# Performance work log

Hardware: AMD Instinct MI355X
Metric: run time of the kernel (lower is better)

Reference implementation:

```python
import jax, jax.numpy as jnp
import numpy as np

N = 100000   # nodes
E = 1600000  # edges (avg degree 16)
H = 128      # hidden_dim
G = 256      # graphs in batch
IN = 2       # input feature dim (GCNConv(2, hidden_dim))


def setup_inputs() -> dict:
    key = jax.random.key(0)
    ks = jax.random.split(key, 12)
    def lin(k, fan_in, shape):
        # kaiming-uniform-ish init, scale irrelevant for correctness testing
        return jax.random.uniform(k, shape, jnp.float32, -1.0, 1.0) / np.sqrt(fan_in).astype(np.float32)
    return {
        "x": jax.random.normal(ks[0], (N, IN), jnp.float32),
        "edge_src": jax.random.randint(ks[1], (E,), 0, N, jnp.int32),
        "edge_dst": jax.random.randint(ks[2], (E,), 0, N, jnp.int32),
        "batch_ids": jnp.sort(jax.random.randint(ks[3], (N,), 0, G, jnp.int32)),
        "num_graphs": G,
        "W1": lin(ks[4], IN, (IN, H)), "b1": jnp.zeros((H,), jnp.float32),
        "W2": lin(ks[5], H, (H, H)),  "b2": jnp.zeros((H,), jnp.float32),
        "fc1_W": lin(ks[6], H, (H, H)), "fc1_b": lin(ks[7], H, (H,)),
        "fc2_W": lin(ks[8], H, (H, 1)), "fc2_b": lin(ks[9], H, (1,)),
    }


def gcn_layer(x, W, b, src, dst, n):
    # PyG GCNConv: add self-loops, symmetric deg^{-1/2} normalization,
    # linear transform, scatter-add aggregation, bias.
    h = x @ W                                                     # [N, H]
    deg = jax.ops.segment_sum(jnp.ones_like(src, jnp.float32), dst, num_segments=n) + 1.0  # +1 self-loop
    dinv = jax.lax.rsqrt(deg)                                     # [N]
    norm = dinv[src] * dinv[dst]                                  # [E]
    agg = jax.ops.segment_sum(h[src] * norm[:, None], dst, num_segments=n)  # [N, H]
    # self-loop contribution: deg_i^{-1/2} * deg_i^{-1/2} = 1/deg_i
    return agg + h * (1.0 / deg)[:, None] + b


def reference(x, edge_src, edge_dst, batch_ids, num_graphs,
              W1, b1, W2, b2, fc1_W, fc1_b, fc2_W, fc2_b):
    n = x.shape[0]
    h = jax.nn.relu(gcn_layer(x, W1, b1, edge_src, edge_dst, n))
    h = jax.nn.relu(gcn_layer(h, W2, b2, edge_src, edge_dst, n))
    # global_mean_pool
    sums = jax.ops.segment_sum(h, batch_ids, num_segments=num_graphs)            # [G, H]
    cnt = jax.ops.segment_sum(jnp.ones((n,), jnp.float32), batch_ids, num_segments=num_graphs)
    pooled = sums / jnp.maximum(cnt, 1.0)[:, None]
    h = jax.nn.relu(pooled @ fc1_W + fc1_b)
    return h @ fc2_W + fc2_b                                                     # [G, 1]
```

## Files before the change

### kernel.cpp

```cpp
#include <hip/hip_runtime.h>
#include <stdint.h>

#define HD 128
#define BSH 9
#define BNODES 512
#define PER 8
#define SCAP 256

typedef float f32x4 __attribute__((ext_vector_type(4)));
typedef float f32x2 __attribute__((ext_vector_type(2)));
typedef short s16x8 __attribute__((ext_vector_type(8)));

static inline int idiv(int a, int b) { return (a + b - 1) / b; }

__device__ __forceinline__ unsigned short f2b(float f) {
  unsigned u = __float_as_uint(f);
  return (unsigned short)((u + 0x7fffu + ((u >> 16) & 1u)) >> 16);
}

__global__ void __launch_bounds__(256) k_cnt(const int* __restrict__ edst,
                                             int* __restrict__ btot,
                                             int E, int NB, int chunk) {
  __shared__ int hist[512];
  int blk = blockIdx.x;
  for (int b = threadIdx.x; b < NB; b += 256) hist[b] = 0;
  __syncthreads();
  int s0 = blk * chunk, s1 = min(E, s0 + chunk);
  for (int k = s0 + threadIdx.x; k < s1; k += 256)
    atomicAdd(&hist[edst[k] >> BSH], 1);
  __syncthreads();
  for (int b = threadIdx.x; b < NB; b += 256) {
    int h = hist[b];
    if (h) atomicAdd(&btot[b], h);
  }
}

__global__ void __launch_bounds__(1024) k_bscan(const int* __restrict__ btot,
                                                int* __restrict__ bstart,
                                                int* __restrict__ gcur,
                                                float4* __restrict__ td,
                                                int NB, int E, int N) {
  __shared__ int sh[1024];
  int t = threadIdx.x;
  int a0 = (2 * t < NB) ? btot[2 * t] : 0;
  int a1 = (2 * t + 1 < NB) ? btot[2 * t + 1] : 0;
  int s = a0 + a1;
  sh[t] = s;
  __syncthreads();
  for (int off = 1; off < 1024; off <<= 1) {
    int add = (t >= off) ? sh[t - off] : 0;
    __syncthreads();
    sh[t] += add;
    __syncthreads();
  }
  int excl = sh[t] - s;
  if (2 * t < NB) { bstart[2 * t] = excl; gcur[2 * t] = excl; }
  if (2 * t + 1 < NB) { bstart[2 * t + 1] = excl + a0; gcur[2 * t + 1] = excl + a0; }
  if (t == 0) {
    bstart[NB] = E;
    td[N] = make_float4(0.f, 0.f, 0.f, 0.f);
  }
}

__global__ void __launch_bounds__(256) k_binscatter2(const int* __restrict__ esrc,
                                                     const int* __restrict__ edst,
                                                     int* __restrict__ gcur,
                                                     unsigned* __restrict__ recs,
                                                     int E, int NB, int chunk) {
  __shared__ int hist[512];
  int blk = blockIdx.x;
  for (int b = threadIdx.x; b < NB; b += 256) hist[b] = 0;
  __syncthreads();
  int s0 = blk * chunk, s1 = min(E, s0 + chunk);
  for (int k = s0 + threadIdx.x; k < s1; k += 256)
    atomicAdd(&hist[edst[k] >> BSH], 1);
  __syncthreads();
  for (int b = threadIdx.x; b < NB; b += 256) {
    int h = hist[b];
    hist[b] = h ? atomicAdd(&gcur[b], h) : 0;
  }
  __syncthreads();
  for (int k = s0 + threadIdx.x; k < s1; k += 256) {
    int d = edst[k], s = esrc[k];
    int b = d >> BSH;
    int pos = atomicAdd(&hist[b], 1);
    recs[pos] = ((unsigned)(d & (BNODES - 1)) << 23) | (unsigned)s;
  }
}

__global__ void __launch_bounds__(256) k_bucketsort(const unsigned* __restrict__ recs,
                                                    const int* __restrict__ bstart,
                                                    const float* __restrict__ x,
                                                    const int* __restrict__ bids,
                                                    unsigned* __restrict__ ssrc16,
                                                    int* __restrict__ row_start,
                                                    int* __restrict__ cnt,
                                                    float* __restrict__ dinv,
                                                    float2* __restrict__ xs,
                                                    int* __restrict__ gstart,
                                                    int NB, int N, int G) {
  __shared__ int count[BNODES], excl[BNODES], cur[BNODES];
  int b = blockIdx.x;
  int t = threadIdx.x;
  for (int d = t; d < BNODES; d += 256) count[d] = 0;
  __syncthreads();
  int rs = bstart[b];
  int re = bstart[b + 1];
  int base_p = rs + b * BNODES;
  for (int k = rs + t; k < re; k += 256) atomicAdd(&count[recs[k] >> 23], 1);
  __syncthreads();
  if (t == 0) {
    int run = 0;
    for (int d = 0; d < BNODES; ++d) { excl[d] = run; run += (count[d] + 1) & ~1; }
  }
  __syncthreads();
  for (int d = t; d < BNODES; d += 256) {
    int i = b * BNODES + d;
    if (i < N) {
      cnt[i] = count[d];
      row_start[i] = base_p + excl[d];
      if (count[d] & 1)
        ssrc16[base_p + excl[d] + count[d]] = (unsigned)N << 4;
      float di = rsqrtf((float)(count[d] + 1));
      dinv[i] = di;
      float2 xv = *(const float2*)&x[2 * i];
      xs[i] = make_float2(di * xv.x, di * xv.y);
      int g = bids[i];
      if (i == 0)
        for (int gg = 0; gg <= g; ++gg) gstart[gg] = 0;
      int gn = (i == N - 1) ? G : bids[i + 1];
      for (int gg = g + 1; gg <= gn; ++gg) gstart[gg] = i + 1;
    }
    cur[d] = excl[d];
  }
  __syncthreads();
  for (int k = rs + t; k < re; k += 256) {
    unsigned r = recs[k];
    int dl = r >> 23;
    int pos = base_p + atomicAdd(&cur[dl], 1);
    ssrc16[pos] = (r & 0x007fffffu) << 4;
  }
}

__global__ void k_aggx2(const int* __restrict__ row_start, const int* __restrict__ cnt,
                        const unsigned* __restrict__ ssrc16, const float2* __restrict__ xs,
                        const float* __restrict__ dinv, float4* __restrict__ td, int N) {
  int i = blockIdx.x * 256 + threadIdx.x;
  if (i >= N) return;
  int rs = row_start[i], re = rs + cnt[i];
  float a0 = 0.f, a1 = 0.f;
  int k = rs;
  for (; k + 1 < re; k += 2) {
    unsigned v0 = ssrc16[k] >> 4, v1 = ssrc16[k + 1] >> 4;
    float2 p0 = xs[v0], p1 = xs[v1];
    a0 += p0.x + p1.x; a1 += p0.y + p1.y;
  }
  if (k < re) {
    float2 p = xs[ssrc16[k] >> 4];
    a0 += p.x; a1 += p.y;
  }
  float2 self = xs[i];
  float di = dinv[i];
  td[i] = make_float4(di * (a0 + self.x), di * (a1 + self.y), di, 0.f);
}

__global__ void __launch_bounds__(256) k_aggh(
    const int* __restrict__ row_start, const int* __restrict__ cnt,
    const unsigned* __restrict__ ssrc16, const float4* __restrict__ td,
    const float* __restrict__ W1, const float* __restrict__ b1,
    unsigned* __restrict__ m_b, int N) {
  __shared__ float4 sbuf[4][SCAP];
  int wave = threadIdx.x >> 6;
  int lane = threadIdx.x & 63;
  int wid = blockIdx.x * 4 + wave;
  int i0 = wid * PER;
  if (i0 >= N) return;
  int nn = min(N - i0, PER);
  int hl = lane >> 5;
  int fq = (lane & 31) * 4;
  f32x4 w0 = *(const f32x4*)&W1[fq];
  f32x4 w1 = *(const f32x4*)&W1[HD + fq];
  f32x4 bb = *(const f32x4*)&b1[fq];
  int mydeg = (lane < nn) ? cnt[i0 + lane] : 0;
  float4 mytd = (lane < nn) ? td[i0 + lane] : make_float4(0.f, 0.f, 0.f, 0.f);
  int mx = __float_as_int(mytd.x), my = __float_as_int(mytd.y), mz = __float_as_int(mytd.z);
  int mypad = (mydeg + 1) & ~1;
  int total = 0;
#pragma unroll
  for (int u = 0; u < PER; ++u) total += __builtin_amdgcn_readlane(mypad, u);
  int rs0 = __builtin_amdgcn_readfirstlane(row_start[i0]);
  const char* tdc = (const char*)td;
  bool staged = (total <= SCAP);
  if (staged) {
#pragma unroll
    for (int w = 0; w < SCAP / 64; ++w) {
      int sl = w * 64 + lane;
      if (sl < total) {
        unsigned off = ssrc16[rs0 + sl];
        sbuf[wave][sl] = *(const float4*)(tdc + off);
      }
    }
  }
  int k = 0;
  const f32x4 zero4 = {0.f, 0.f, 0.f, 0.f};
  for (int node = 0; node < nn; ++node) {
    int deg = __builtin_amdgcn_readlane(mydeg, node);
    int np = (deg + 1) >> 1;
    f32x4 acc = zero4;
    if (staged) {
#pragma unroll 2
      for (int p = 0; p < np; ++p) {
        float4 t = sbuf[wave][k + 2 * p + hl];
        f32x4 h = f32x4{t.y, t.y, t.y, t.y} * w1 + bb;
        h = f32x4{t.x, t.x, t.x, t.x} * w0 + h;
        h = __builtin_elementwise_max(h, zero4);
        acc = f32x4{t.z, t.z, t.z, t.z} * h + acc;
      }
    } else {
      for (int p = 0; p < np; ++p) {
        unsigned off = ssrc16[rs0 + k + 2 * p + hl];
        float4 t = *(const float4*)(tdc + off);
        f32x4 h = f32x4{t.y, t.y, t.y, t.y} * w1 + bb;
        h = f32x4{t.x, t.x, t.x, t.x} * w0 + h;
        h = __builtin_elementwise_max(h, zero4);
        acc = f32x4{t.z, t.z, t.z, t.z} * h + acc;
      }
    }
    k += np * 2;
    f32x4 tot;
#pragma unroll
    for (int c = 0; c < 4; ++c) tot[c] = acc[c] + __shfl_xor(acc[c], 32);
    float tx = __int_as_float(__builtin_amdgcn_readlane(mx, node));
    float ty = __int_as_float(__builtin_amdgcn_readlane(my, node));
    float tz = __int_as_float(__builtin_amdgcn_readlane(mz, node));
    f32x4 h = f32x4{ty, ty, ty, ty} * w1 + bb;
    h = f32x4{tx, tx, tx, tx} * w0 + h;
    h = __builtin_elementwise_max(h, zero4);
    f32x4 r = f32x4{tz, tz, tz, tz} * h + tot;
    float v0 = (hl ? r[2] : r[0]) * tz;
    float v1 = (hl ? r[3] : r[1]) * tz;
    int j = hl ? (2 * (lane - 32) + 1) : (2 * lane);
    m_b[(unsigned)(i0 + node) * 64 + j] = ((unsigned)f2b(v1) << 16) | f2b(v0);
  }
}

__global__ void k_w2t(const float* __restrict__ W2, unsigned* __restrict__ w2f,
                      int* __restrict__ btot, int NB) {
  int f = blockIdx.x * 256 + threadIdx.x;
  if (f < NB) btot[f] = 0;
  if (f >= 2048) return;
  int c = f >> 8, s = (f >> 6) & 3, lane = f & 63;
  int col = c * 16 + (lane & 15);
  int kb = s * 32 + (lane >> 4) * 8;
  unsigned hi4[4], lo4[4];
#pragma unroll
  for (int j = 0; j < 4; ++j) {
    float w0 = W2[(kb + 2 * j) * HD + col];
    float w1 = W2[(kb + 2 * j + 1) * HD + col];
    unsigned short h0 = f2b(w0), h1 = f2b(w1);
    float r0 = w0 - __uint_as_float((unsigned)h0 << 16);
    float r1 = w1 - __uint_as_float((unsigned)h1 << 16);
    unsigned short l0 = f2b(r0), l1 = f2b(r1);
    hi4[j] = ((unsigned)h1 << 16) | h0;
    lo4[j] = ((unsigned)l1 << 16) | l0;
  }
  *(uint4*)&w2f[f * 4] = make_uint4(hi4[0], hi4[1], hi4[2], hi4[3]);
  *(uint4*)&w2f[8192 + f * 4] = make_uint4(lo4[0], lo4[1], lo4[2], lo4[3]);
}

__global__ void __launch_bounds__(256) k_t2pool(
    const unsigned* __restrict__ m_b, const unsigned* __restrict__ w2f,
    const float* __restrict__ b2, const int* __restrict__ gstart,
    const float* __restrict__ fc1W, const float* __restrict__ fc1b,
    const float* __restrict__ fc2W, const float* __restrict__ fc2b,
    float* __restrict__ out, int N, int G) {
  __shared__ unsigned W[16384];
  __shared__ float pool[16][HD];
  __shared__ float ps[HD];
  __shared__ float rsh[HD];
  int g = blockIdx.x;
  for (int u = threadIdx.x; u < 4096; u += 256)
    *(uint4*)&W[u * 4] = *(const uint4*)&w2f[u * 4];
  for (int u = threadIdx.x; u < 16 * HD; u += 256) ((float*)pool)[u] = 0.f;
  const int lane = threadIdx.x & 63;
  const int wave = threadIdx.x >> 6;
  const int col = lane & 15;
  const int kg = lane >> 4;
  float bb[8];
#pragma unroll
  for (int c = 0; c < 8; ++c) bb[c] = b2[c * 16 + col];
  int s0 = gstart[g], e0 = gstart[g + 1];
  int ntiles = (e0 - s0 + 15) >> 4;
  float pacc[8];
#pragma unroll
  for (int c = 0; c < 8; ++c) pacc[c] = 0.f;
  __syncthreads();
  for (int tile = wave; tile < ntiles; tile += 4) {
    int rbase = s0 + tile * 16;
    int arow = rbase + col;
    if (arow >= N) arow = N - 1;
    f32x4 acc[8];
#pragma unroll
    for (int c = 0; c < 8; ++c) acc[c] = f32x4{0.f, 0.f, 0.f, 0.f};
#pragma unroll
    for (int s = 0; s < 4; ++s) {
      uint4 av = *(const uint4*)&m_b[((size_t)arow << 6) + s * 16 + kg * 4];
      s16x8 A = *(s16x8*)&av;
#pragma unroll
      for (int c = 0; c < 8; ++c) {
        int f = (c * 4 + s) * 64 + lane;
        s16x8 Bh = *(s16x8*)&W[f * 4];
        s16x8 Bl = *(s16x8*)&W[8192 + f * 4];
        acc[c] = __builtin_amdgcn_mfma_f32_16x16x32_bf16(A, Bh, acc[c], 0, 0, 0);
        acc[c] = __builtin_amdgcn_mfma_f32_16x16x32_bf16(A, Bl, acc[c], 0, 0, 0);
      }
    }
    int orow = rbase + kg * 4;
#pragma unroll
    for (int c = 0; c < 8; ++c) {
#pragma unroll
      for (int r = 0; r < 4; ++r) {
        if (orow + r < e0) pacc[c] += fmaxf(acc[c][r] + bb[c], 0.f);
      }
    }
  }
#pragma unroll
  for (int c = 0; c < 8; ++c) pool[wave * 4 + kg][c * 16 + col] = pacc[c];
  __syncthreads();
  int j = threadIdx.x;
  if (j < HD) {
    float a = 0.f;
#pragma unroll
    for (int r = 0; r < 16; ++r) a += pool[r][j];
    float cg = (float)(e0 - s0);
    cg = cg < 1.f ? 1.f : cg;
    ps[j] = a / cg;
  }
  __syncthreads();
  if (j < HD) {
    float a = fc1b[j];
#pragma unroll 4
    for (int k = 0; k < HD; ++k) a = fmaf(ps[k], fc1W[k * HD + j], a);
    rsh[j] = fmaxf(a, 0.f) * fc2W[j];
  }
  __syncthreads();
  for (int off = 64; off > 0; off >>= 1) {
    if (j < off) rsh[j] += rsh[j + off];
    __syncthreads();
  }
  if (j == 0) out[g] = rsh[0] + fc2b[0];
}

extern "C" void kernel_launch(void* const* d_in, const int* in_sizes, int n_in,
                              void* d_out, int out_size, void* d_ws, size_t ws_size,
                              hipStream_t stream) {
  const float* x    = (const float*)d_in[0];
  const int* esrc   = (const int*)d_in[1];
  const int* edst   = (const int*)d_in[2];
  const int* bids   = (const int*)d_in[3];
  const float* W1   = (const float*)d_in[5];
  const float* b1   = (const float*)d_in[6];
  const float* W2   = (const float*)d_in[7];
  const float* b2   = (const float*)d_in[8];
  const float* fc1W = (const float*)d_in[9];
  const float* fc1b = (const float*)d_in[10];
  const float* fc2W = (const float*)d_in[11];
  const float* fc2b = (const float*)d_in[12];
  float* out = (float*)d_out;

  const int N = in_sizes[0] / 2;
  const int E = in_sizes[1];
  const int G = out_size;

  const int NB = idiv(N, BNODES);
  const int chunk = idiv(E, 256);

  char* w = (char*)d_ws;
  size_t o = 0;
  auto take = [&](size_t b) -> char* {
    char* p = w + o;
    o = (o + b + 255) & ~(size_t)255;
    return p;
  };
  int*      btot      = (int*)     take((size_t)NB * 4);
  int*      bstart    = (int*)     take((size_t)(NB + 1) * 4);
  int*      gcur      = (int*)     take((size_t)NB * 4);
  unsigned* recs      = (unsigned*)take((size_t)E * 4);
  unsigned* ssrc16    = (unsigned*)take((size_t)(E + (size_t)NB * BNODES + 128) * 4);
  int*      cnt       = (int*)     take((size_t)N * 4);
  int*      row_start = (int*)     take((size_t)N * 4);
  float*    dinv      = (float*)   take((size_t)N * 4);
  float*    xs        = (float*)   take((size_t)N * 8);
  float*    td        = (float*)   take((size_t)(N + 1) * 16);
  int*      gstart    = (int*)     take((size_t)(G + 1) * 4);
  unsigned* m_b       = (unsigned*)take((size_t)N * 64 * 4);
  unsigned* w2f       = (unsigned*)take(16384 * 4);

  k_w2t<<<8, 256, 0, stream>>>(W2, w2f, btot, NB);
  k_cnt<<<256, 256, 0, stream>>>(edst, btot, E, NB, chunk);
  k_bscan<<<1, 1024, 0, stream>>>(btot, bstart, gcur, (float4*)td, NB, E, N);
  k_binscatter2<<<256, 256, 0, stream>>>(esrc, edst, gcur, recs, E, NB, chunk);
  k_bucketsort<<<NB, 256, 0, stream>>>(recs, bstart, x, bids, ssrc16, row_start,
                                       cnt, dinv, (float2*)xs, gstart, NB, N, G);
  k_aggx2<<<idiv(N, 256), 256, 0, stream>>>(row_start, cnt, ssrc16, (const float2*)xs,
                                            dinv, (float4*)td, N);
  int waves = idiv(N, PER);
  k_aggh<<<idiv(waves, 4), 256, 0, stream>>>(row_start, cnt, ssrc16, (const float4*)td,
                                             W1, b1, m_b, N);
  k_t2pool<<<G, 256, 0, stream>>>(m_b, w2f, b2, gstart, fc1W, fc1b, fc2W, fc2b, out, N, G);
}
```

Before: 144.4 us.

## Parallelize bucket prefix scan, unroll layer-1 gather, double binning block count

The per-bucket exclusive scan in the bucket sort, which ran serially on one thread over 512 entries, becomes a two-level scan: 64 threads each sum 8 entries and a single thread scans the 64 partial sums. The first-layer gather loop is unrolled by four with two independent accumulator pairs, giving more loads in flight. The edge counting and binning kernels launch 512 blocks instead of 256 on smaller chunks to fill more compute units. More blocks means more global atomics on the bucket counters, and the reordered float sums change rounding slightly.

After: 141.5 us. 1.02x faster.

```diff
diff --git a/kernel.cpp b/kernel.cpp
--- a/kernel.cpp
+++ b/kernel.cpp
@@ -6,6 +6,7 @@
 #define BNODES 512
 #define PER 8
 #define SCAP 256
+#define BINBLK 512
 
 typedef float f32x4 __attribute__((ext_vector_type(4)));
 typedef float f32x2 __attribute__((ext_vector_type(2)));
@@ -99,7 +100,7 @@
                                                     float2* __restrict__ xs,
                                                     int* __restrict__ gstart,
                                                     int NB, int N, int G) {
-  __shared__ int count[BNODES], excl[BNODES], cur[BNODES];
+  __shared__ int count[BNODES], excl[BNODES], cur[BNODES], psum[64];
   int b = blockIdx.x;
   int t = threadIdx.x;
   for (int d = t; d < BNODES; d += 256) count[d] = 0;
@@ -109,9 +110,25 @@
   int base_p = rs + b * BNODES;
   for (int k = rs + t; k < re; k += 256) atomicAdd(&count[recs[k] >> 23], 1);
   __syncthreads();
+  if (t < 64) {
+    int s = 0;
+#pragma unroll
+    for (int u = 0; u < 8; ++u) s += (count[t * 8 + u] + 1) & ~1;
+    psum[t] = s;
+  }
+  __syncthreads();
   if (t == 0) {
     int run = 0;
-    for (int d = 0; d < BNODES; ++d) { excl[d] = run; run += (count[d] + 1) & ~1; }
+    for (int d = 0; d < 64; ++d) { int v = psum[d]; psum[d] = run; run += v; }
+  }
+  __syncthreads();
+  if (t < 64) {
+    int run = psum[t];
+#pragma unroll
+    for (int u = 0; u < 8; ++u) {
+      excl[t * 8 + u] = run;
+      run += (count[t * 8 + u] + 1) & ~1;
+    }
   }
   __syncthreads();
   for (int d = t; d < BNODES; d += 256) {
@@ -148,17 +165,20 @@
   int i = blockIdx.x * 256 + threadIdx.x;
   if (i >= N) return;
   int rs = row_start[i], re = rs + cnt[i];
-  float a0 = 0.f, a1 = 0.f;
+  float a0 = 0.f, a1 = 0.f, b0 = 0.f, b1 = 0.f;
   int k = rs;
-  for (; k + 1 < re; k += 2) {
+  for (; k + 3 < re; k += 4) {
     unsigned v0 = ssrc16[k] >> 4, v1 = ssrc16[k + 1] >> 4;
-    float2 p0 = xs[v0], p1 = xs[v1];
+    unsigned v2 = ssrc16[k + 2] >> 4, v3 = ssrc16[k + 3] >> 4;
+    float2 p0 = xs[v0], p1 = xs[v1], p2 = xs[v2], p3 = xs[v3];
     a0 += p0.x + p1.x; a1 += p0.y + p1.y;
-  }
-  if (k < re) {
+    b0 += p2.x + p3.x; b1 += p2.y + p3.y;
+  }
+  for (; k < re; ++k) {
     float2 p = xs[ssrc16[k] >> 4];
     a0 += p.x; a1 += p.y;
   }
+  a0 += b0; a1 += b1;
   float2 self = xs[i];
   float di = dinv[i];
   td[i] = make_float4(di * (a0 + self.x), di * (a1 + self.y), di, 0.f);
@@ -373,7 +393,7 @@
   const int G = out_size;
 
   const int NB = idiv(N, BNODES);
-  const int chunk = idiv(E, 256);
+  const int chunk = idiv(E, BINBLK);
 
   char* w = (char*)d_ws;
   size_t o = 0;
@@ -397,9 +417,9 @@
   unsigned* w2f       = (unsigned*)take(16384 * 4);
 
   k_w2t<<<8, 256, 0, stream>>>(W2, w2f, btot, NB);
-  k_cnt<<<256, 256, 0, stream>>>(edst, btot, E, NB, chunk);
+  k_cnt<<<BINBLK, 256, 0, stream>>>(edst, btot, E, NB, chunk);
   k_bscan<<<1, 1024, 0, stream>>>(btot, bstart, gcur, (float4*)td, NB, E, N);
-  k_binscatter2<<<256, 256, 0, stream>>>(esrc, edst, gcur, recs, E, NB, chunk);
+  k_binscatter2<<<BINBLK, 256, 0, stream>>>(esrc, edst, gcur, recs, E, NB, chunk);
   k_bucketsort<<<NB, 256, 0, stream>>>(recs, bstart, x, bids, ssrc16, row_start,
                                        cnt, dinv, (float2*)xs, gstart, NB, N, G);
   k_aggx2<<<idiv(N, 256), 256, 0, stream>>>(row_start, cnt, ssrc16, (const float2*)xs,
```
